# Optimization experiments

Hardware: AMD Instinct MI355X
Metric: run time of the kernel (lower is better)

The kernel has to match this reference:

```python
import jax, jax.numpy as jnp
import numpy as np


def gcn_conv(x, edge_index, W, b):
    """PyG GCNConv with default add_self_loops=True, normalize=True.

    edge_index[0] = source (j), edge_index[1] = target (i), flow source_to_target.
    norm = deg^{-1/2}[j] * deg^{-1/2}[i], deg computed on target col with
    self-loops included (edge weight 1).
    """
    N = x.shape[0]
    loops = jnp.arange(N, dtype=edge_index.dtype)
    row = jnp.concatenate([edge_index[0], loops])  # sources j
    col = jnp.concatenate([edge_index[1], loops])  # targets i

    ones = jnp.ones(row.shape[0], dtype=x.dtype)
    deg = jax.ops.segment_sum(ones, col, num_segments=N)  # [N]
    deg_inv_sqrt = jnp.where(deg > 0, jax.lax.rsqrt(deg), 0.0)
    norm = deg_inv_sqrt[row] * deg_inv_sqrt[col]  # [E+N]

    h = x @ W  # [N, out] linear transform before propagation
    msg = norm[:, None] * h[row]  # gather from sources
    out = jax.ops.segment_sum(msg, col, num_segments=N)  # scatter-add to targets
    return out + b


def setup_inputs() -> dict:
    key = jax.random.key(0)
    k1, k2, k3, k4 = jax.random.split(key, 4)
    N, E = 100000, 1600000
    d_in, d_hid, d_out = 128, 128, 64
    x = jax.random.normal(k1, (N, d_in), dtype=jnp.float32)
    edge_index = jax.random.randint(k2, (2, E), 0, N, dtype=jnp.int32)
    # Glorot-ish init for weights
    W1 = jax.random.normal(k3, (d_in, d_hid), dtype=jnp.float32) / np.sqrt(d_in)
    b1 = jnp.zeros((d_hid,), dtype=jnp.float32)
    W2 = jax.random.normal(k4, (d_hid, d_out), dtype=jnp.float32) / np.sqrt(d_hid)
    b2 = jnp.zeros((d_out,), dtype=jnp.float32)
    return {"x": x, "edge_index": edge_index, "W1": W1, "b1": b1, "W2": W2, "b2": b2}


def reference(x, edge_index, W1, b1, W2, b2):
    h = gcn_conv(x, edge_index, W1, b1)
    h = jax.nn.relu(h)
    out = gcn_conv(h, edge_index, W2, b2)
    return out
```

## Files before the change

kernel.cpp:

```cpp
#include <hip/hip_runtime.h>

typedef unsigned int uint;
typedef unsigned short ushort;
typedef short s8v __attribute__((ext_vector_type(8)));
typedef float f4v __attribute__((ext_vector_type(4)));

#define BSHIFT 8
#define NBUCK_MAX 512
#define PART_CH 8192
#define DBINS 128
#define GS_CH 2048


__device__ __forceinline__ uint f2bf(float f) {
    uint b = __float_as_uint(f);
    return (b + 0x7fffu + ((b >> 16) & 1u)) >> 16;
}
__device__ __forceinline__ uint pack2(float a, float b) {
    return f2bf(a) | (f2bf(b) << 16);
}
__device__ __forceinline__ float bflo(uint u) { return __uint_as_float(u << 16); }
__device__ __forceinline__ float bfhi(uint u) { return __uint_as_float(u & 0xffff0000u); }


__global__ __launch_bounds__(256) void hist_k(const int* __restrict__ dst, int E, int nbuck,
                                              int* __restrict__ bcnt) {
    __shared__ int h[NBUCK_MAX];
    int t = threadIdx.x;
    for (int i = t; i < nbuck; i += 256) h[i] = 0;
    __syncthreads();
    int e0 = blockIdx.x * PART_CH;
    int e1 = min(e0 + PART_CH, E);
    for (int e = e0 + t; e < e1; e += 256) atomicAdd(&h[((uint)dst[e]) >> BSHIFT], 1);
    __syncthreads();
    for (int i = t; i < nbuck; i += 256) {
        int v = h[i];
        if (v) atomicAdd(&bcnt[i], v);
    }
}

__global__ __launch_bounds__(512) void bscan_k(const int* __restrict__ bcnt, int nbuck, int E,
                                               int* __restrict__ bo, int* __restrict__ bcur) {
    __shared__ int s[512];
    int t = threadIdx.x;
    int v = (t < nbuck) ? bcnt[t] : 0;
    s[t] = v;
    __syncthreads();
    for (int off = 1; off < 512; off <<= 1) {
        int x = (t >= off) ? s[t - off] : 0;
        __syncthreads();
        s[t] += x;
        __syncthreads();
    }
    int excl = s[t] - v;
    if (t < nbuck) { bo[t] = excl; bcur[t] = excl; }
    if (t == 0) bo[nbuck] = E;
}

__global__ __launch_bounds__(256) void part_k(const int* __restrict__ src,
                                              const int* __restrict__ dst, int E, int nbuck,
                                              int* __restrict__ bcur, uint* __restrict__ eb) {
    __shared__ int h[NBUCK_MAX];
    __shared__ int cur[NBUCK_MAX];
    int t = threadIdx.x;
    for (int i = t; i < nbuck; i += 256) h[i] = 0;
    __syncthreads();
    int e0 = blockIdx.x * PART_CH;
    int e1 = min(e0 + PART_CH, E);
    for (int e = e0 + t; e < e1; e += 256) atomicAdd(&h[((uint)dst[e]) >> BSHIFT], 1);
    __syncthreads();
    for (int i = t; i < nbuck; i += 256) {
        int v = h[i];
        cur[i] = v ? atomicAdd(&bcur[i], v) : 0;
    }
    __syncthreads();
    for (int e = e0 + t; e < e1; e += 256) {
        int d = dst[e];
        int b = ((uint)d) >> BSHIFT;
        int p = atomicAdd(&cur[b], 1);
        eb[p] = ((uint)src[e] << BSHIFT) | (uint)(d & 255);
    }
}

__global__ __launch_bounds__(256) void build_k(const uint* __restrict__ eb,
                                               const int* __restrict__ bo, int N, int E,
                                               int* __restrict__ rowptr,
                                               int* __restrict__ csr) {
    __shared__ int c[256];
    __shared__ int s[256];
    int b = blockIdx.x;
    int t = threadIdx.x;
    int node0 = b << BSHIFT;
    int beg = bo[b], end = bo[b + 1];
    c[t] = 0;
    __syncthreads();
    for (int e = beg + t; e < end; e += 256) atomicAdd(&c[eb[e] & 255], 1);
    __syncthreads();
    int v = c[t];
    s[t] = v;
    __syncthreads();
    for (int off = 1; off < 256; off <<= 1) {
        int x = (t >= off) ? s[t - off] : 0;
        __syncthreads();
        s[t] += x;
        __syncthreads();
    }
    int excl = s[t] - v;
    int node = node0 + t;
    if (node < N) rowptr[node] = beg + excl;
    if (b == 0 && t == 0) rowptr[N] = E;
    __syncthreads();
    c[t] = beg + excl;
    __syncthreads();
    for (int e = beg + t; e < end; e += 256) {
        uint pk = eb[e];
        int p = atomicAdd(&c[pk & 255], 1);
        csr[p] = (int)(pk >> BSHIFT);
    }
}


__global__ void dinv_k(const int* __restrict__ rowptr, float* __restrict__ dinv, int N) {
    int i = blockIdx.x * blockDim.x + threadIdx.x;
    if (i < N) dinv[i] = rsqrtf((float)(1 + rowptr[i + 1] - rowptr[i]));
}


__global__ __launch_bounds__(256) void gs1_k(const int* __restrict__ in, int M,
                                             int* __restrict__ bs) {
    __shared__ int sd[256];
    int base = blockIdx.x * GS_CH;
    int sum = 0;
    for (int i = threadIdx.x; i < GS_CH; i += 256) {
        int idx = base + i;
        if (idx < M) sum += in[idx];
    }
    sd[threadIdx.x] = sum;
    __syncthreads();
    for (int s = 128; s > 0; s >>= 1) {
        if (threadIdx.x < s) sd[threadIdx.x] += sd[threadIdx.x + s];
        __syncthreads();
    }
    if (threadIdx.x == 0) bs[blockIdx.x] = sd[0];
}

__global__ __launch_bounds__(512) void gs2_k(int* __restrict__ bs, int nb) {
    __shared__ int s[512];
    int t = threadIdx.x;
    int v = (t < nb) ? bs[t] : 0;
    s[t] = v;
    __syncthreads();
    for (int off = 1; off < 512; off <<= 1) {
        int x = (t >= off) ? s[t - off] : 0;
        __syncthreads();
        s[t] += x;
        __syncthreads();
    }
    if (t < nb) bs[t] = s[t] - v;
}

__global__ __launch_bounds__(256) void gs3_k(const int* __restrict__ in, int M,
                                             const int* __restrict__ bs, int* __restrict__ out) {
    __shared__ int s[256];
    int base = blockIdx.x * GS_CH;
    int t = threadIdx.x;
    int loc[8];
    int sum = 0;
#pragma unroll
    for (int i = 0; i < 8; ++i) {
        int idx = base + t * 8 + i;
        int c = (idx < M) ? in[idx] : 0;
        loc[i] = sum;
        sum += c;
    }
    s[t] = sum;
    __syncthreads();
    int inc = sum;
    for (int off = 1; off < 256; off <<= 1) {
        int x = (t >= off) ? s[t - off] : 0;
        __syncthreads();
        s[t] += x;
        __syncthreads();
    }
    int toff = s[t] - inc + bs[blockIdx.x];
#pragma unroll
    for (int i = 0; i < 8; ++i) {
        int idx = base + t * 8 + i;
        if (idx < M) out[idx] = toff + loc[i];
    }
}


__global__ __launch_bounds__(256) void dhist2_k(const int* __restrict__ rowptr, int N, int NBLK,
                                                int* __restrict__ dh_blk) {
    __shared__ int h[DBINS];
    int t = threadIdx.x;
    if (t < DBINS) h[t] = 0;
    __syncthreads();
    int i = blockIdx.x * 256 + t;
    if (i < N) atomicAdd(&h[min(rowptr[i + 1] - rowptr[i], DBINS - 1)], 1);
    __syncthreads();
    if (t < DBINS) dh_blk[t * NBLK + blockIdx.x] = h[t];
}

__global__ __launch_bounds__(256) void dplace2_k(const int* __restrict__ rowptr, int N, int NBLK,
                                                 const int* __restrict__ dhoff,
                                                 int* __restrict__ perm, int2* __restrict__ rp2) {
    __shared__ int cur[DBINS];
    int t = threadIdx.x;
    int blk = blockIdx.x;
    if (t < DBINS) cur[t] = 0;
    __syncthreads();
    int i = blk * 256 + t;
    int bin = 0, beg = 0, end = 0, rank = 0;
    if (i < N) {
        beg = rowptr[i];
        end = rowptr[i + 1];
        bin = min(end - beg, DBINS - 1);
        rank = atomicAdd(&cur[bin], 1);
    }
    __syncthreads();
    if (t < DBINS) cur[t] = dhoff[t * NBLK + blk];
    __syncthreads();
    if (i < N) {
        int pos = cur[bin] + rank;
        perm[pos] = i;
        rp2[pos] = make_int2(beg, end);
    }
}


template <int OUTC>
__global__ void wtrans_k(const float* __restrict__ W, ushort* __restrict__ Wt) {
    int c = blockIdx.x * 64 + threadIdx.x;
    if (c >= OUTC) return;
    for (int k0 = 0; k0 < 128; k0 += 8) {
        float v[8];
#pragma unroll
        for (int i = 0; i < 8; ++i) v[i] = W[(size_t)(k0 + i) * OUTC + c];
        uint4 p;
        p.x = pack2(v[0], v[1]);
        p.y = pack2(v[2], v[3]);
        p.z = pack2(v[4], v[5]);
        p.w = pack2(v[6], v[7]);
        *(uint4*)(Wt + (size_t)c * 128 + k0) = p;
    }
}


template <int OUTC, bool AF32>
__global__ __launch_bounds__(256) void gemm_mfma(const void* __restrict__ Ain,
                                                 const ushort* __restrict__ Wt,
                                                 const float* __restrict__ dinv,
                                                 ushort* __restrict__ hs, int N) {
    constexpr int NT = OUTC / 16;
    constexpr int LDK = 136;
    __shared__ ushort Al[64 * LDK];
    __shared__ ushort Wl[OUTC * LDK];

    int tid = threadIdx.x;
    int row0 = blockIdx.x * 64;

    {
        int r = tid >> 2, seg = tid & 3;
        int gr = row0 + r;
        if (gr > N - 1) gr = N - 1;
        ushort* dstp = &Al[r * LDK + seg * 32];
        if (AF32) {
            const float4* ap = (const float4*)((const float*)Ain + (size_t)gr * 128 + seg * 32);
#pragma unroll
            for (int i = 0; i < 4; ++i) {
                float4 f0 = ap[2 * i], f1 = ap[2 * i + 1];
                uint4 u;
                u.x = pack2(f0.x, f0.y);
                u.y = pack2(f0.z, f0.w);
                u.z = pack2(f1.x, f1.y);
                u.w = pack2(f1.z, f1.w);
                *(uint4*)(dstp + i * 8) = u;
            }
        } else {
            const uint4* ap = (const uint4*)((const ushort*)Ain + (size_t)gr * 128 + seg * 32);
#pragma unroll
            for (int i = 0; i < 4; ++i) *(uint4*)(dstp + i * 8) = ap[i];
        }
    }
    {
        const uint4* wp = (const uint4*)Wt;
        for (int idx = tid; idx < OUTC * 16; idx += 256) {
            int r = idx >> 4, c = idx & 15;
            *(uint4*)(&Wl[r * LDK + c * 8]) = wp[idx];
        }
    }
    __syncthreads();

    int w = tid >> 6;
    int l = tid & 63;
    int lo = l & 15, q = l >> 4;

    f4v acc[NT];
#pragma unroll
    for (int i = 0; i < NT; ++i) acc[i] = (f4v){0.f, 0.f, 0.f, 0.f};

#pragma unroll
    for (int ks = 0; ks < 4; ++ks) {
        s8v af = *(const s8v*)&Al[(16 * w + lo) * LDK + ks * 32 + q * 8];
#pragma unroll
        for (int nt = 0; nt < NT; ++nt) {
            s8v wf = *(const s8v*)&Wl[(nt * 16 + lo) * LDK + ks * 32 + q * 8];
            acc[nt] = __builtin_amdgcn_mfma_f32_16x16x32_bf16(wf, af, acc[nt], 0, 0, 0);
        }
    }

    int grow = row0 + 16 * w + lo;
    if (grow < N) {
        float dr = dinv[grow];
        ushort* orow = hs + (size_t)grow * OUTC + q * 4;
#pragma unroll
        for (int nt = 0; nt < NT; ++nt) {
            uint2 p;
            p.x = pack2(acc[nt][0] * dr, acc[nt][1] * dr);
            p.y = pack2(acc[nt][2] * dr, acc[nt][3] * dr);
            *(uint2*)(orow + nt * 16) = p;
        }
    }
}


template <int C, bool RELU, bool OUTBF>
__global__ __launch_bounds__(256) void aggregate_p(const ushort* __restrict__ hs,
                                                   const int* __restrict__ perm,
                                                   const int2* __restrict__ rp2,
                                                   const int* __restrict__ csr,
                                                   const float* __restrict__ bias,
                                                   void* __restrict__ out, int N) {
    constexpr int LANES = C / 8;
    constexpr int NPB = 256 / LANES;
    int tid = threadIdx.x;
    int sub = tid / LANES;
    int lane = tid % LANES;
    int pos = blockIdx.x * NPB + sub;
    if (pos >= N) return;
    int node = perm[pos];
    int2 rp = rp2[pos];
    float di = rsqrtf((float)(1 + rp.y - rp.x));

    const uint4* h4 = (const uint4*)hs;
    float accA[8], accB[8];
    {
        uint4 v = h4[(size_t)node * LANES + lane];
        accA[0] = bflo(v.x); accA[1] = bfhi(v.x);
        accA[2] = bflo(v.y); accA[3] = bfhi(v.y);
        accA[4] = bflo(v.z); accA[5] = bfhi(v.z);
        accA[6] = bflo(v.w); accA[7] = bfhi(v.w);
    }
#pragma unroll
    for (int k = 0; k < 8; ++k) accB[k] = 0.f;

    int e = rp.x, end = rp.y;
    for (; e + 8 <= end; e += 8) {
        int j[8];
#pragma unroll
        for (int k = 0; k < 8; ++k) j[k] = csr[e + k];
        uint4 v[8];
#pragma unroll
        for (int k = 0; k < 8; ++k) v[k] = h4[(size_t)j[k] * LANES + lane];
#pragma unroll
        for (int k = 0; k < 8; ++k) {
            float* a = (k & 1) ? accB : accA;
            a[0] += bflo(v[k].x); a[1] += bfhi(v[k].x);
            a[2] += bflo(v[k].y); a[3] += bfhi(v[k].y);
            a[4] += bflo(v[k].z); a[5] += bfhi(v[k].z);
            a[6] += bflo(v[k].w); a[7] += bfhi(v[k].w);
        }
    }
    if (e + 4 <= end) {
        int j0 = csr[e], j1 = csr[e + 1], j2 = csr[e + 2], j3 = csr[e + 3];
        uint4 v0 = h4[(size_t)j0 * LANES + lane];
        uint4 v1 = h4[(size_t)j1 * LANES + lane];
        uint4 v2 = h4[(size_t)j2 * LANES + lane];
        uint4 v3 = h4[(size_t)j3 * LANES + lane];
        accA[0] += bflo(v0.x) + bflo(v2.x); accA[1] += bfhi(v0.x) + bfhi(v2.x);
        accA[2] += bflo(v0.y) + bflo(v2.y); accA[3] += bfhi(v0.y) + bfhi(v2.y);
        accA[4] += bflo(v0.z) + bflo(v2.z); accA[5] += bfhi(v0.z) + bfhi(v2.z);
        accA[6] += bflo(v0.w) + bflo(v2.w); accA[7] += bfhi(v0.w) + bfhi(v2.w);
        accB[0] += bflo(v1.x) + bflo(v3.x); accB[1] += bfhi(v1.x) + bfhi(v3.x);
        accB[2] += bflo(v1.y) + bflo(v3.y); accB[3] += bfhi(v1.y) + bfhi(v3.y);
        accB[4] += bflo(v1.z) + bflo(v3.z); accB[5] += bfhi(v1.z) + bfhi(v3.z);
        accB[6] += bflo(v1.w) + bflo(v3.w); accB[7] += bfhi(v1.w) + bfhi(v3.w);
        e += 4;
    }
    for (; e < end; ++e) {
        int j = csr[e];
        uint4 v = h4[(size_t)j * LANES + lane];
        accA[0] += bflo(v.x); accA[1] += bfhi(v.x);
        accA[2] += bflo(v.y); accA[3] += bfhi(v.y);
        accA[4] += bflo(v.z); accA[5] += bfhi(v.z);
        accA[6] += bflo(v.w); accA[7] += bfhi(v.w);
    }

    const float4* b4 = (const float4*)(bias + lane * 8);
    float4 b0 = b4[0], b1 = b4[1];
    float o[8];
    o[0] = fmaf(di, accA[0] + accB[0], b0.x);
    o[1] = fmaf(di, accA[1] + accB[1], b0.y);
    o[2] = fmaf(di, accA[2] + accB[2], b0.z);
    o[3] = fmaf(di, accA[3] + accB[3], b0.w);
    o[4] = fmaf(di, accA[4] + accB[4], b1.x);
    o[5] = fmaf(di, accA[5] + accB[5], b1.y);
    o[6] = fmaf(di, accA[6] + accB[6], b1.z);
    o[7] = fmaf(di, accA[7] + accB[7], b1.w);
    if (RELU) {
#pragma unroll
        for (int k = 0; k < 8; ++k) o[k] = fmaxf(o[k], 0.f);
    }
    if (OUTBF) {
        uint4 p;
        p.x = pack2(o[0], o[1]);
        p.y = pack2(o[2], o[3]);
        p.z = pack2(o[4], o[5]);
        p.w = pack2(o[6], o[7]);
        *(uint4*)((ushort*)out + (size_t)node * C + lane * 8) = p;
    } else {
        float* op = (float*)out + (size_t)node * C + lane * 8;
        *(float4*)op = make_float4(o[0], o[1], o[2], o[3]);
        *(float4*)(op + 4) = make_float4(o[4], o[5], o[6], o[7]);
    }
}


extern "C" void kernel_launch(void* const* d_in, const int* in_sizes, int n_in,
                              void* d_out, int out_size, void* d_ws, size_t ws_size,
                              hipStream_t stream) {
    const float* x  = (const float*)d_in[0];
    const int*   ei = (const int*)d_in[1];
    const float* W1 = (const float*)d_in[2];
    const float* b1 = (const float*)d_in[3];
    const float* W2 = (const float*)d_in[4];
    const float* b2 = (const float*)d_in[5];
    float* out = (float*)d_out;

    const int D = 128;
    int N = in_sizes[0] / D;
    int E = in_sizes[1] / 2;
    const int* src = ei;
    const int* dst = ei + E;

    int nbuck = (N + 255) >> BSHIFT;
    int NBLK = (N + 255) / 256;

    char* ws = (char*)d_ws;
    size_t off = 0;
    auto alloc = [&](size_t bytes) -> void* {
        void* p = ws + off;
        off += (bytes + 255) & ~(size_t)255;
        return p;
    };
    int*    bcnt  = (int*)alloc((size_t)NBUCK_MAX * 4);
    int*    bo    = (int*)alloc((size_t)(NBUCK_MAX + 1) * 4);
    int*    bcur  = (int*)alloc((size_t)NBUCK_MAX * 4);
    int*    rowptr= (int*)alloc((size_t)(N + 1) * 4);
    int*    dh_blk= (int*)alloc((size_t)DBINS * NBLK * 4);
    int*    dhoff = (int*)alloc((size_t)DBINS * NBLK * 4);
    int*    gb    = (int*)alloc(2048);
    float*  dinv  = (float*)alloc((size_t)N * 4);
    int*    perm  = (int*)alloc((size_t)N * 4);
    int2*   rp2   = (int2*)alloc((size_t)N * 8);
    uint*   eb    = (uint*)alloc((size_t)E * 4);
    int*    csr   = (int*)alloc((size_t)E * 4);
    ushort* wt1   = (ushort*)alloc((size_t)128 * 128 * 2);
    ushort* wt2   = (ushort*)alloc((size_t)64 * 128 * 2);
    ushort* hs1   = (ushort*)alloc((size_t)N * 128 * 2);
    ushort* h1a   = (ushort*)alloc((size_t)N * 128 * 2);
    ushort* hs2   = hs1;

    int PB = (E + PART_CH - 1) / PART_CH;
    int M1 = DBINS * NBLK;
    int G1 = (M1 + GS_CH - 1) / GS_CH;

    hipMemsetAsync(bcnt, 0, (size_t)NBUCK_MAX * 4, stream);
    hist_k<<<PB, 256, 0, stream>>>(dst, E, nbuck, bcnt);
    bscan_k<<<1, 512, 0, stream>>>(bcnt, nbuck, E, bo, bcur);
    part_k<<<PB, 256, 0, stream>>>(src, dst, E, nbuck, bcur, eb);
    build_k<<<nbuck, 256, 0, stream>>>(eb, bo, N, E, rowptr, csr);
    dinv_k<<<NBLK, 256, 0, stream>>>(rowptr, dinv, N);
    dhist2_k<<<NBLK, 256, 0, stream>>>(rowptr, N, NBLK, dh_blk);
    gs1_k<<<G1, 256, 0, stream>>>(dh_blk, M1, gb);
    gs2_k<<<1, 512, 0, stream>>>(gb, G1);
    gs3_k<<<G1, 256, 0, stream>>>(dh_blk, M1, gb, dhoff);
    dplace2_k<<<NBLK, 256, 0, stream>>>(rowptr, N, NBLK, dhoff, perm, rp2);
    wtrans_k<128><<<2, 64, 0, stream>>>(W1, wt1);
    wtrans_k<64><<<1, 64, 0, stream>>>(W2, wt2);

    int gG = (N + 63) / 64;
    gemm_mfma<128, true><<<gG, 256, 0, stream>>>(x, wt1, dinv, hs1, N);
    aggregate_p<128, true, true><<<(N + 15) / 16, 256, 0, stream>>>(hs1, perm, rp2, csr, b1, h1a, N);
    gemm_mfma<64, false><<<gG, 256, 0, stream>>>(h1a, wt2, dinv, hs2, N);
    aggregate_p<64, false, false><<<(N + 31) / 32, 256, 0, stream>>>(hs2, perm, rp2, csr, b2, out, N);
}
```

Baseline: 226.5 us.

## Fuse layer-1 aggregation with layer-2 GEMM and drop degree-sort permutation

```diff
diff --git a/kernel.cpp b/kernel.cpp
--- a/kernel.cpp
+++ b/kernel.cpp
@@ -8,7 +8,6 @@
 #define BSHIFT 8
 #define NBUCK_MAX 512
 #define PART_CH 8192
-#define DBINS 128
 #define GS_CH 2048
 
 
@@ -23,8 +22,8 @@
 __device__ __forceinline__ float bfhi(uint u) { return __uint_as_float(u & 0xffff0000u); }
 
 
-__global__ __launch_bounds__(256) void hist_k(const int* __restrict__ dst, int E, int nbuck,
-                                              int* __restrict__ bcnt) {
+__global__ __launch_bounds__(256) void hist2_k(const int* __restrict__ dst, int E, int nbuck,
+                                               int PB, int* __restrict__ cnt_blk) {
     __shared__ int h[NBUCK_MAX];
     int t = threadIdx.x;
     for (int i = t; i < nbuck; i += 256) h[i] = 0;
@@ -33,17 +32,32 @@
     int e1 = min(e0 + PART_CH, E);
     for (int e = e0 + t; e < e1; e += 256) atomicAdd(&h[((uint)dst[e]) >> BSHIFT], 1);
     __syncthreads();
-    for (int i = t; i < nbuck; i += 256) {
-        int v = h[i];
-        if (v) atomicAdd(&bcnt[i], v);
-    }
-}
-
-__global__ __launch_bounds__(512) void bscan_k(const int* __restrict__ bcnt, int nbuck, int E,
-                                               int* __restrict__ bo, int* __restrict__ bcur) {
+    for (int i = t; i < nbuck; i += 256) cnt_blk[i * PB + blockIdx.x] = h[i];
+}
+
+
+__global__ __launch_bounds__(256) void gs1_k(const int* __restrict__ in, int M,
+                                             int* __restrict__ bs) {
+    __shared__ int sd[256];
+    int base = blockIdx.x * GS_CH;
+    int sum = 0;
+    for (int i = threadIdx.x; i < GS_CH; i += 256) {
+        int idx = base + i;
+        if (idx < M) sum += in[idx];
+    }
+    sd[threadIdx.x] = sum;
+    __syncthreads();
+    for (int s = 128; s > 0; s >>= 1) {
+        if (threadIdx.x < s) sd[threadIdx.x] += sd[threadIdx.x + s];
+        __syncthreads();
+    }
+    if (threadIdx.x == 0) bs[blockIdx.x] = sd[0];
+}
+
+__global__ __launch_bounds__(512) void gs2_k(int* __restrict__ bs, int nb) {
     __shared__ int s[512];
     int t = threadIdx.x;
-    int v = (t < nbuck) ? bcnt[t] : 0;
+    int v = (t < nb) ? bs[t] : 0;
     s[t] = v;
     __syncthreads();
     for (int off = 1; off < 512; off <<= 1) {
@@ -52,28 +66,58 @@
         s[t] += x;
         __syncthreads();
     }
-    int excl = s[t] - v;
-    if (t < nbuck) { bo[t] = excl; bcur[t] = excl; }
-    if (t == 0) bo[nbuck] = E;
-}
-
-__global__ __launch_bounds__(256) void part_k(const int* __restrict__ src,
-                                              const int* __restrict__ dst, int E, int nbuck,
-                                              int* __restrict__ bcur, uint* __restrict__ eb) {
-    __shared__ int h[NBUCK_MAX];
+    if (t < nb) bs[t] = s[t] - v;
+}
+
+__global__ __launch_bounds__(256) void gs3_k(const int* __restrict__ in, int M,
+                                             const int* __restrict__ bs, int* __restrict__ out) {
+    __shared__ int s[256];
+    int base = blockIdx.x * GS_CH;
+    int t = threadIdx.x;
+    int loc[8];
+    int sum = 0;
+#pragma unroll
+    for (int i = 0; i < 8; ++i) {
+        int idx = base + t * 8 + i;
+        int c = (idx < M) ? in[idx] : 0;
+        loc[i] = sum;
+        sum += c;
+    }
+    s[t] = sum;
+    __syncthreads();
+    int inc = sum;
+    for (int off = 1; off < 256; off <<= 1) {
+        int x = (t >= off) ? s[t - off] : 0;
+        __syncthreads();
+        s[t] += x;
+        __syncthreads();
+    }
+    int toff = s[t] - inc + bs[blockIdx.x];
+#pragma unroll
+    for (int i = 0; i < 8; ++i) {
+        int idx = base + t * 8 + i;
+        if (idx < M) out[idx] = toff + loc[i];
+    }
+}
+
+__global__ void boext_k(const int* __restrict__ off_blk, int nbuck, int PB, int E,
+                        int* __restrict__ bo) {
+    int i = blockIdx.x * blockDim.x + threadIdx.x;
+    if (i < nbuck) bo[i] = off_blk[i * PB];
+    if (i == 0) bo[nbuck] = E;
+}
+
+__global__ __launch_bounds__(256) void part2_k(const int* __restrict__ src,
+                                               const int* __restrict__ dst, int E, int nbuck,
+                                               int PB, const int* __restrict__ off_blk,
+                                               uint* __restrict__ eb) {
     __shared__ int cur[NBUCK_MAX];
     int t = threadIdx.x;
-    for (int i = t; i < nbuck; i += 256) h[i] = 0;
-    __syncthreads();
-    int e0 = blockIdx.x * PART_CH;
+    int blk = blockIdx.x;
+    for (int i = t; i < nbuck; i += 256) cur[i] = off_blk[i * PB + blk];
+    __syncthreads();
+    int e0 = blk * PART_CH;
     int e1 = min(e0 + PART_CH, E);
-    for (int e = e0 + t; e < e1; e += 256) atomicAdd(&h[((uint)dst[e]) >> BSHIFT], 1);
-    __syncthreads();
-    for (int i = t; i < nbuck; i += 256) {
-        int v = h[i];
-        cur[i] = v ? atomicAdd(&bcur[i], v) : 0;
-    }
-    __syncthreads();
     for (int e = e0 + t; e < e1; e += 256) {
         int d = dst[e];
         int b = ((uint)d) >> BSHIFT;
@@ -119,114 +163,9 @@
     }
 }
 
-
 __global__ void dinv_k(const int* __restrict__ rowptr, float* __restrict__ dinv, int N) {
     int i = blockIdx.x * blockDim.x + threadIdx.x;
     if (i < N) dinv[i] = rsqrtf((float)(1 + rowptr[i + 1] - rowptr[i]));
-}
-
-
-__global__ __launch_bounds__(256) void gs1_k(const int* __restrict__ in, int M,
-                                             int* __restrict__ bs) {
-    __shared__ int sd[256];
-    int base = blockIdx.x * GS_CH;
-    int sum = 0;
-    for (int i = threadIdx.x; i < GS_CH; i += 256) {
-        int idx = base + i;
-        if (idx < M) sum += in[idx];
-    }
-    sd[threadIdx.x] = sum;
-    __syncthreads();
-    for (int s = 128; s > 0; s >>= 1) {
-        if (threadIdx.x < s) sd[threadIdx.x] += sd[threadIdx.x + s];
-        __syncthreads();
-    }
-    if (threadIdx.x == 0) bs[blockIdx.x] = sd[0];
-}
-
-__global__ __launch_bounds__(512) void gs2_k(int* __restrict__ bs, int nb) {
-    __shared__ int s[512];
-    int t = threadIdx.x;
-    int v = (t < nb) ? bs[t] : 0;
-    s[t] = v;
-    __syncthreads();
-    for (int off = 1; off < 512; off <<= 1) {
-        int x = (t >= off) ? s[t - off] : 0;
-        __syncthreads();
-        s[t] += x;
-        __syncthreads();
-    }
-    if (t < nb) bs[t] = s[t] - v;
-}
-
-__global__ __launch_bounds__(256) void gs3_k(const int* __restrict__ in, int M,
-                                             const int* __restrict__ bs, int* __restrict__ out) {
-    __shared__ int s[256];
-    int base = blockIdx.x * GS_CH;
-    int t = threadIdx.x;
-    int loc[8];
-    int sum = 0;
-#pragma unroll
-    for (int i = 0; i < 8; ++i) {
-        int idx = base + t * 8 + i;
-        int c = (idx < M) ? in[idx] : 0;
-        loc[i] = sum;
-        sum += c;
-    }
-    s[t] = sum;
-    __syncthreads();
-    int inc = sum;
-    for (int off = 1; off < 256; off <<= 1) {
-        int x = (t >= off) ? s[t - off] : 0;
-        __syncthreads();
-        s[t] += x;
-        __syncthreads();
-    }
-    int toff = s[t] - inc + bs[blockIdx.x];
-#pragma unroll
-    for (int i = 0; i < 8; ++i) {
-        int idx = base + t * 8 + i;
-        if (idx < M) out[idx] = toff + loc[i];
-    }
-}
-
-
-__global__ __launch_bounds__(256) void dhist2_k(const int* __restrict__ rowptr, int N, int NBLK,
-                                                int* __restrict__ dh_blk) {
-    __shared__ int h[DBINS];
-    int t = threadIdx.x;
-    if (t < DBINS) h[t] = 0;
-    __syncthreads();
-    int i = blockIdx.x * 256 + t;
-    if (i < N) atomicAdd(&h[min(rowptr[i + 1] - rowptr[i], DBINS - 1)], 1);
-    __syncthreads();
-    if (t < DBINS) dh_blk[t * NBLK + blockIdx.x] = h[t];
-}
-
-__global__ __launch_bounds__(256) void dplace2_k(const int* __restrict__ rowptr, int N, int NBLK,
-                                                 const int* __restrict__ dhoff,
-                                                 int* __restrict__ perm, int2* __restrict__ rp2) {
-    __shared__ int cur[DBINS];
-    int t = threadIdx.x;
-    int blk = blockIdx.x;
-    if (t < DBINS) cur[t] = 0;
-    __syncthreads();
-    int i = blk * 256 + t;
-    int bin = 0, beg = 0, end = 0, rank = 0;
-    if (i < N) {
-        beg = rowptr[i];
-        end = rowptr[i + 1];
-        bin = min(end - beg, DBINS - 1);
-        rank = atomicAdd(&cur[bin], 1);
-    }
-    __syncthreads();
-    if (t < DBINS) cur[t] = dhoff[t * NBLK + blk];
-    __syncthreads();
-    if (i < N) {
-        int pos = cur[bin] + rank;
-        perm[pos] = i;
-        rp2[pos] = make_int2(beg, end);
-    }
 }
 
 
@@ -326,10 +265,142 @@
 }
 
 
+__global__ __launch_bounds__(256) void agg1_fused_k(const ushort* __restrict__ hs,
+                                                    const float* __restrict__ dinv,
+                                                    const int* __restrict__ rowptr,
+                                                    const int* __restrict__ csr,
+                                                    const float* __restrict__ b1,
+                                                    const ushort* __restrict__ wt2,
+                                                    ushort* __restrict__ hs2, int N) {
+    constexpr int LDK2 = 136;
+    __shared__ ushort rows[16 * LDK2];
+    __shared__ ushort Wl2[64 * LDK2];
+    __shared__ float dinvv[16];
+
+    int tid = threadIdx.x;
+    {
+        const uint4* wp = (const uint4*)wt2;
+        for (int idx = tid; idx < 64 * 16; idx += 256) {
+            int r = idx >> 4, c = idx & 15;
+            *(uint4*)(&Wl2[r * LDK2 + c * 8]) = wp[idx];
+        }
+    }
+
+    int sub = tid >> 4;
+    int lane = tid & 15;
+    int node = blockIdx.x * 16 + sub;
+    bool valid = node < N;
+
+    const uint4* h4 = (const uint4*)hs;
+    float accA[8], accB[8];
+#pragma unroll
+    for (int k = 0; k < 8; ++k) { accA[k] = 0.f; accB[k] = 0.f; }
+    float di = 0.f;
+    int e = 0, end = 0;
+    if (valid) {
+        di = dinv[node];
+        e = rowptr[node];
+        end = rowptr[node + 1];
+        uint4 v = h4[(size_t)node * 16 + lane];
+        accA[0] = bflo(v.x); accA[1] = bfhi(v.x);
+        accA[2] = bflo(v.y); accA[3] = bfhi(v.y);
+        accA[4] = bflo(v.z); accA[5] = bfhi(v.z);
+        accA[6] = bflo(v.w); accA[7] = bfhi(v.w);
+    }
+
+    for (; e + 8 <= end; e += 8) {
+        int j[8];
+#pragma unroll
+        for (int k = 0; k < 8; ++k) j[k] = csr[e + k];
+        uint4 v[8];
+#pragma unroll
+        for (int k = 0; k < 8; ++k) v[k] = h4[(size_t)j[k] * 16 + lane];
+#pragma unroll
+        for (int k = 0; k < 8; ++k) {
+            float* a = (k & 1) ? accB : accA;
+            a[0] += bflo(v[k].x); a[1] += bfhi(v[k].x);
+            a[2] += bflo(v[k].y); a[3] += bfhi(v[k].y);
+            a[4] += bflo(v[k].z); a[5] += bfhi(v[k].z);
+            a[6] += bflo(v[k].w); a[7] += bfhi(v[k].w);
+        }
+    }
+    if (e + 4 <= end) {
+        int j0 = csr[e], j1 = csr[e + 1], j2 = csr[e + 2], j3 = csr[e + 3];
+        uint4 v0 = h4[(size_t)j0 * 16 + lane];
+        uint4 v1 = h4[(size_t)j1 * 16 + lane];
+        uint4 v2 = h4[(size_t)j2 * 16 + lane];
+        uint4 v3 = h4[(size_t)j3 * 16 + lane];
+        accA[0] += bflo(v0.x) + bflo(v2.x); accA[1] += bfhi(v0.x) + bfhi(v2.x);
+        accA[2] += bflo(v0.y) + bflo(v2.y); accA[3] += bfhi(v0.y) + bfhi(v2.y);
+        accA[4] += bflo(v0.z) + bflo(v2.z); accA[5] += bfhi(v0.z) + bfhi(v2.z);
+        accA[6] += bflo(v0.w) + bflo(v2.w); accA[7] += bfhi(v0.w) + bfhi(v2.w);
+        accB[0] += bflo(v1.x) + bflo(v3.x); accB[1] += bfhi(v1.x) + bfhi(v3.x);
+        accB[2] += bflo(v1.y) + bflo(v3.y); accB[3] += bfhi(v1.y) + bfhi(v3.y);
+        accB[4] += bflo(v1.z) + bflo(v3.z); accB[5] += bfhi(v1.z) + bfhi(v3.z);
+        accB[6] += bflo(v1.w) + bflo(v3.w); accB[7] += bfhi(v1.w) + bfhi(v3.w);
+        e += 4;
+    }
+    for (; e < end; ++e) {
+        uint4 v = h4[(size_t)csr[e] * 16 + lane];
+        accA[0] += bflo(v.x); accA[1] += bfhi(v.x);
+        accA[2] += bflo(v.y); accA[3] += bfhi(v.y);
+        accA[4] += bflo(v.z); accA[5] += bfhi(v.z);
+        accA[6] += bflo(v.w); accA[7] += bfhi(v.w);
+    }
+
+    float o[8];
+    if (valid) {
+        const float4* b4 = (const float4*)(b1 + lane * 8);
+        float4 bb0 = b4[0], bb1 = b4[1];
+        o[0] = fmaxf(fmaf(di, accA[0] + accB[0], bb0.x), 0.f);
+        o[1] = fmaxf(fmaf(di, accA[1] + accB[1], bb0.y), 0.f);
+        o[2] = fmaxf(fmaf(di, accA[2] + accB[2], bb0.z), 0.f);
+        o[3] = fmaxf(fmaf(di, accA[3] + accB[3], bb0.w), 0.f);
+        o[4] = fmaxf(fmaf(di, accA[4] + accB[4], bb1.x), 0.f);
+        o[5] = fmaxf(fmaf(di, accA[5] + accB[5], bb1.y), 0.f);
+        o[6] = fmaxf(fmaf(di, accA[6] + accB[6], bb1.z), 0.f);
+        o[7] = fmaxf(fmaf(di, accA[7] + accB[7], bb1.w), 0.f);
+    } else {
+#pragma unroll
+        for (int k = 0; k < 8; ++k) o[k] = 0.f;
+    }
+
+    {
+        uint4 p;
+        p.x = pack2(o[0], o[1]);
+        p.y = pack2(o[2], o[3]);
+        p.z = pack2(o[4], o[5]);
+        p.w = pack2(o[6], o[7]);
+        *(uint4*)(&rows[sub * LDK2 + lane * 8]) = p;
+        if (lane == 0) dinvv[sub] = di;
+    }
+    __syncthreads();
+
+    int w = tid >> 6;
+    int l = tid & 63;
+    int lo = l & 15, q = l >> 4;
+    f4v acc = (f4v){0.f, 0.f, 0.f, 0.f};
+#pragma unroll
+    for (int ks = 0; ks < 4; ++ks) {
+        s8v af = *(const s8v*)&rows[lo * LDK2 + ks * 32 + q * 8];
+        s8v wf = *(const s8v*)&Wl2[(w * 16 + lo) * LDK2 + ks * 32 + q * 8];
+        acc = __builtin_amdgcn_mfma_f32_16x16x32_bf16(wf, af, acc, 0, 0, 0);
+    }
+    int gn = blockIdx.x * 16 + lo;
+    if (gn < N) {
+        float dr = dinvv[lo];
+        uint2 p;
+        p.x = pack2(acc[0] * dr, acc[1] * dr);
+        p.y = pack2(acc[2] * dr, acc[3] * dr);
+        *(uint2*)(hs2 + (size_t)gn * 64 + w * 16 + q * 4) = p;
+    }
+}
+
+
 template <int C, bool RELU, bool OUTBF>
-__global__ __launch_bounds__(256) void aggregate_p(const ushort* __restrict__ hs,
-                                                   const int* __restrict__ perm,
-                                                   const int2* __restrict__ rp2,
+__global__ __launch_bounds__(256) void aggregate_k(const ushort* __restrict__ hs,
+                                                   const float* __restrict__ dinv,
+                                                   const int* __restrict__ rowptr,
                                                    const int* __restrict__ csr,
                                                    const float* __restrict__ bias,
                                                    void* __restrict__ out, int N) {
@@ -338,11 +409,8 @@
     int tid = threadIdx.x;
     int sub = tid / LANES;
     int lane = tid % LANES;
-    int pos = blockIdx.x * NPB + sub;
-    if (pos >= N) return;
-    int node = perm[pos];
-    int2 rp = rp2[pos];
-    float di = rsqrtf((float)(1 + rp.y - rp.x));
+    int node = blockIdx.x * NPB + sub;
+    if (node >= N) return;
 
     const uint4* h4 = (const uint4*)hs;
     float accA[8], accB[8];
@@ -356,7 +424,9 @@
 #pragma unroll
     for (int k = 0; k < 8; ++k) accB[k] = 0.f;
 
-    int e = rp.x, end = rp.y;
+    int e = rowptr[node];
+    int end = rowptr[node + 1];
+    float di = dinv[node];
     for (; e + 8 <= end; e += 8) {
         int j[8];
 #pragma unroll
@@ -390,8 +460,7 @@
         e += 4;
     }
     for (; e < end; ++e) {
-        int j = csr[e];
-        uint4 v = h4[(size_t)j * LANES + lane];
+        uint4 v = h4[(size_t)csr[e] * LANES + lane];
         accA[0] += bflo(v.x); accA[1] += bfhi(v.x);
         accA[2] += bflo(v.y); accA[3] += bfhi(v.y);
         accA[4] += bflo(v.z); accA[5] += bfhi(v.z);
@@ -447,6 +516,9 @@
 
     int nbuck = (N + 255) >> BSHIFT;
     int NBLK = (N + 255) / 256;
+    int PB = (E + PART_CH - 1) / PART_CH;
+    int M1 = nbuck * PB;
+    int G1 = (M1 + GS_CH - 1) / GS_CH;
 
     char* ws = (char*)d_ws;
     size_t off = 0;
@@ -455,45 +527,31 @@
         off += (bytes + 255) & ~(size_t)255;
         return p;
     };
-    int*    bcnt  = (int*)alloc((size_t)NBUCK_MAX * 4);
-    int*    bo    = (int*)alloc((size_t)(NBUCK_MAX + 1) * 4);
-    int*    bcur  = (int*)alloc((size_t)NBUCK_MAX * 4);
-    int*    rowptr= (int*)alloc((size_t)(N + 1) * 4);
-    int*    dh_blk= (int*)alloc((size_t)DBINS * NBLK * 4);
-    int*    dhoff = (int*)alloc((size_t)DBINS * NBLK * 4);
-    int*    gb    = (int*)alloc(2048);
-    float*  dinv  = (float*)alloc((size_t)N * 4);
-    int*    perm  = (int*)alloc((size_t)N * 4);
-    int2*   rp2   = (int2*)alloc((size_t)N * 8);
-    uint*   eb    = (uint*)alloc((size_t)E * 4);
-    int*    csr   = (int*)alloc((size_t)E * 4);
-    ushort* wt1   = (ushort*)alloc((size_t)128 * 128 * 2);
-    ushort* wt2   = (ushort*)alloc((size_t)64 * 128 * 2);
-    ushort* hs1   = (ushort*)alloc((size_t)N * 128 * 2);
-    ushort* h1a   = (ushort*)alloc((size_t)N * 128 * 2);
-    ushort* hs2   = hs1;
-
-    int PB = (E + PART_CH - 1) / PART_CH;
-    int M1 = DBINS * NBLK;
-    int G1 = (M1 + GS_CH - 1) / GS_CH;
-
-    hipMemsetAsync(bcnt, 0, (size_t)NBUCK_MAX * 4, stream);
-    hist_k<<<PB, 256, 0, stream>>>(dst, E, nbuck, bcnt);
-    bscan_k<<<1, 512, 0, stream>>>(bcnt, nbuck, E, bo, bcur);
-    part_k<<<PB, 256, 0, stream>>>(src, dst, E, nbuck, bcur, eb);
+    int*    cnt_blk = (int*)alloc((size_t)M1 * 4);
+    int*    off_blk = (int*)alloc((size_t)M1 * 4);
+    int*    gb      = (int*)alloc(2048);
+    int*    bo      = (int*)alloc((size_t)(NBUCK_MAX + 1) * 4);
+    int*    rowptr  = (int*)alloc((size_t)(N + 1) * 4);
+    float*  dinv    = (float*)alloc((size_t)N * 4);
+    uint*   eb      = (uint*)alloc((size_t)E * 4);
+    int*    csr     = (int*)alloc((size_t)E * 4);
+    ushort* wt1     = (ushort*)alloc((size_t)128 * 128 * 2);
+    ushort* wt2     = (ushort*)alloc((size_t)64 * 128 * 2);
+    ushort* hs1     = (ushort*)alloc((size_t)N * 128 * 2);
+    ushort* hs2     = (ushort*)alloc((size_t)N * 64 * 2);
+
+    hist2_k<<<PB, 256, 0, stream>>>(dst, E, nbuck, PB, cnt_blk);
+    gs1_k<<<G1, 256, 0, stream>>>(cnt_blk, M1, gb);
+    gs2_k<<<1, 512, 0, stream>>>(gb, G1);
+    gs3_k<<<G1, 256, 0, stream>>>(cnt_blk, M1, gb, off_blk);
+    boext_k<<<(nbuck + 255) / 256, 256, 0, stream>>>(off_blk, nbuck, PB, E, bo);
+    part2_k<<<PB, 256, 0, stream>>>(src, dst, E, nbuck, PB, off_blk, eb);
     build_k<<<nbuck, 256, 0, stream>>>(eb, bo, N, E, rowptr, csr);
     dinv_k<<<NBLK, 256, 0, stream>>>(rowptr, dinv, N);
-    dhist2_k<<<NBLK, 256, 0, stream>>>(rowptr, N, NBLK, dh_blk);
-    gs1_k<<<G1, 256, 0, stream>>>(dh_blk, M1, gb);
-    gs2_k<<<1, 512, 0, stream>>>(gb, G1);
-    gs3_k<<<G1, 256, 0, stream>>>(dh_blk, M1, gb, dhoff);
-    dplace2_k<<<NBLK, 256, 0, stream>>>(rowptr, N, NBLK, dhoff, perm, rp2);
     wtrans_k<128><<<2, 64, 0, stream>>>(W1, wt1);
     wtrans_k<64><<<1, 64, 0, stream>>>(W2, wt2);
 
-    int gG = (N + 63) / 64;
-    gemm_mfma<128, true><<<gG, 256, 0, stream>>>(x, wt1, dinv, hs1, N);
-    aggregate_p<128, true, true><<<(N + 15) / 16, 256, 0, stream>>>(hs1, perm, rp2, csr, b1, h1a, N);
-    gemm_mfma<64, false><<<gG, 256, 0, stream>>>(h1a, wt2, dinv, hs2, N);
-    aggregate_p<64, false, false><<<(N + 31) / 32, 256, 0, stream>>>(hs2, perm, rp2, csr, b2, out, N);
-}
+    gemm_mfma<128, true><<<(N + 63) / 64, 256, 0, stream>>>(x, wt1, dinv, hs1, N);
+    agg1_fused_k<<<(N + 15) / 16, 256, 0, stream>>>(hs1, dinv, rowptr, csr, b1, wt2, hs2, N);
+    aggregate_k<64, false, false><<<(N + 31) / 32, 256, 0, stream>>>(hs2, dinv, rowptr, csr, b2, out, N);
+}
```

After: 199.8 us. 1.13x faster.
